# Optimization experiments

Measured on AMD Instinct MI355X. Metric: run time of the kernel, lower is better.

Reference implementation:

```python
import math
import jax, jax.numpy as jnp
import numpy as np

N = 50000      # num nodes
E = 400000     # num edges
IN = 128       # in_channels
HID = 64       # hidden_channels
HEADS = 4
OUT = 32       # out_channels
TDIM = 16      # time_dim
NEG_SLOPE = 0.2
EPS = 1e-5


def setup_inputs() -> dict:
    key = jax.random.key(0)
    ks = jax.random.split(key, 20)
    s = 0.05
    # Fourier time encoder: Linear(1, TDIM) with freq-pattern weight
    freq = np.exp(np.arange(0, TDIM, 2, dtype=np.float32) * -(math.log(10000.0) / TDIM))
    tw = np.zeros((TDIM,), dtype=np.float32)
    tw[0::2] = freq
    tw[1::2] = freq
    return {
        "x": jax.random.normal(ks[0], (N, IN), jnp.float32),
        "edge_index": jax.random.randint(ks[1], (2, E), 0, N, jnp.int64),
        "edge_time": jax.random.uniform(ks[2], (E,), jnp.float32),
        "time_w": jnp.asarray(tw),
        "time_b": jax.random.normal(ks[3], (TDIM,), jnp.float32) * s,
        "proj_w": jax.random.normal(ks[4], (IN + TDIM, IN), jnp.float32) * s,
        "proj_b": jax.random.normal(ks[5], (IN,), jnp.float32) * s,
        "W1": jax.random.normal(ks[6], (IN, HEADS * HID), jnp.float32) * s,
        "a_src1": jax.random.normal(ks[7], (HEADS, HID), jnp.float32) * s,
        "a_dst1": jax.random.normal(ks[8], (HEADS, HID), jnp.float32) * s,
        "b1": jax.random.normal(ks[9], (HEADS * HID,), jnp.float32) * s,
        "g1": jnp.ones((HEADS * HID,), jnp.float32),
        "be1": jnp.zeros((HEADS * HID,), jnp.float32),
        "W2": jax.random.normal(ks[10], (HEADS * HID, OUT), jnp.float32) * s,
        "a_src2": jax.random.normal(ks[11], (1, OUT), jnp.float32) * s,
        "a_dst2": jax.random.normal(ks[12], (1, OUT), jnp.float32) * s,
        "b2": jax.random.normal(ks[13], (OUT,), jnp.float32) * s,
        "g2": jnp.ones((OUT,), jnp.float32),
        "be2": jnp.zeros((OUT,), jnp.float32),
    }


def layer_norm(h, g, b):
    mu = jnp.mean(h, axis=-1, keepdims=True)
    var = jnp.mean(jnp.square(h - mu), axis=-1, keepdims=True)
    return (h - mu) * jax.lax.rsqrt(var + EPS) * g + b


def gat_conv(x, src, dst, W, a_src, a_dst, bias, heads, ch, concat):
    """PyG GATConv (self-loops pre-appended in src/dst), inference (no dropout)."""
    n = x.shape[0]
    h = (x @ W).reshape(n, heads, ch)                       # [N,H,C]
    al_s = jnp.sum(h * a_src, axis=-1)                      # [N,H]
    al_d = jnp.sum(h * a_dst, axis=-1)                      # [N,H]
    e = al_s[src] + al_d[dst]                               # [Etot,H]
    e = jnp.where(e > 0, e, NEG_SLOPE * e)                  # leaky_relu
    m = jax.ops.segment_max(e, dst, num_segments=n)         # scatter-softmax
    ex = jnp.exp(e - m[dst])
    denom = jax.ops.segment_sum(ex, dst, num_segments=n)
    alpha = ex / denom[dst]                                 # [Etot,H]
    out = jax.ops.segment_sum(h[src] * alpha[:, :, None], dst, num_segments=n)  # [N,H,C]
    out = out.reshape(n, heads * ch) if concat else jnp.mean(out, axis=1)
    return out + bias


def reference(x, edge_index, edge_time, time_w, time_b, proj_w, proj_b,
              W1, a_src1, a_dst1, b1, g1, be1,
              W2, a_src2, a_dst2, b2, g2, be2):
    src, dst = edge_index[0], edge_index[1]
    # Fourier time encoding of edge timestamps
    tp = edge_time[:, None] * time_w + time_b               # [E,TDIM]
    even = (jnp.arange(TDIM) % 2) == 0
    t_enc = jnp.where(even, jnp.sin(tp), jnp.cos(tp))       # [E,TDIM]
    # scatter_reduce_(mean, include_self=True) onto source nodes: sum/(count+1)
    t_sum = jax.ops.segment_sum(t_enc, src, num_segments=N)
    cnt = jax.ops.segment_sum(jnp.ones((E,), x.dtype), src, num_segments=N)
    node_time = t_sum / (cnt + 1.0)[:, None]
    xin = jnp.concatenate([x, node_time], axis=-1) @ proj_w + proj_b  # [N,IN]
    # add self loops (PyG GATConv default)
    loop = jnp.arange(N, dtype=src.dtype)
    src2 = jnp.concatenate([src, loop])
    dst2 = jnp.concatenate([dst, loop])
    h = gat_conv(xin, src2, dst2, W1, a_src1, a_dst1, b1, HEADS, HID, True)
    h = jax.nn.elu(h)
    h = layer_norm(h, g1, be1)
    h = gat_conv(h, src2, dst2, W2, a_src2, a_dst2, b2, 1, OUT, False)
    h = layer_norm(h, g2, be2)
    return h
```

## Files before the change

kernel.cpp:

```cpp
#include <hip/hip_runtime.h>
#include <math.h>

#define NN 50000
#define EE 400000
#define INC 128
#define TD 16
#define H1C 256
#define OUTC 32
#define NEG 0.2f
#define PAD 64

typedef _Float16 f16;
typedef __attribute__((ext_vector_type(8))) _Float16 f16x8;
typedef __attribute__((ext_vector_type(2))) _Float16 f16x2;
typedef __attribute__((ext_vector_type(4))) float f32x4;

__device__ __forceinline__ float leaky(float x) { return x > 0.f ? x : NEG * x; }
__device__ __forceinline__ float sel4f(const float4& v, int h) {
  return h == 0 ? v.x : h == 1 ? v.y : h == 2 ? v.z : v.w;
}

__global__ void k_rank(const int* __restrict__ ei, const float* __restrict__ et,
                       int* __restrict__ deg_dst, int* __restrict__ deg_src,
                       int* __restrict__ src_pad, float* __restrict__ et_pad,
                       const float* __restrict__ W1, const float* __restrict__ pw,
                       const float* __restrict__ W2, f16* __restrict__ W1T,
                       f16* __restrict__ pwT, f16* __restrict__ W2T) {
  int gid = blockIdx.x * 256 + threadIdx.x;
  if (gid < EE / 4) {
    int4 sv = *(const int4*)(ei + gid * 4);
    int4 dv = *(const int4*)(ei + EE + gid * 4);
    float4 tv = *(const float4*)(et + gid * 4);
    int rd0 = atomicAdd(&deg_dst[dv.x], 1);
    int rd1 = atomicAdd(&deg_dst[dv.y], 1);
    int rd2 = atomicAdd(&deg_dst[dv.z], 1);
    int rd3 = atomicAdd(&deg_dst[dv.w], 1);
    int rs0 = atomicAdd(&deg_src[sv.x], 1);
    int rs1 = atomicAdd(&deg_src[sv.y], 1);
    int rs2 = atomicAdd(&deg_src[sv.z], 1);
    int rs3 = atomicAdd(&deg_src[sv.w], 1);
    if (rd0 < PAD) src_pad[dv.x * PAD + rd0] = sv.x;
    if (rd1 < PAD) src_pad[dv.y * PAD + rd1] = sv.y;
    if (rd2 < PAD) src_pad[dv.z * PAD + rd2] = sv.z;
    if (rd3 < PAD) src_pad[dv.w * PAD + rd3] = sv.w;
    if (rs0 < PAD) et_pad[sv.x * PAD + rs0] = tv.x;
    if (rs1 < PAD) et_pad[sv.y * PAD + rs1] = tv.y;
    if (rs2 < PAD) et_pad[sv.z * PAD + rs2] = tv.z;
    if (rs3 < PAD) et_pad[sv.w * PAD + rs3] = tv.w;
    return;
  }
  int idx = gid - EE / 4;
  if (idx < 32768) {
    int c = idx >> 7, k = idx & 127;
    W1T[idx] = (f16)W1[k * 256 + c];
  } else if (idx < 53248) {
    int i2 = idx - 32768;
    int c = i2 / 160, kp = i2 - c * 160;
    pwT[i2] = (f16)(kp < 144 ? pw[kp * 128 + c] : 0.f);
  } else if (idx < 61440) {
    int i3 = idx - 53248;
    int c = i3 >> 8, k = i3 & 255;
    W2T[i3] = (f16)W2[k * 32 + c];
  }
}

__global__ void k_time_agg(const int* __restrict__ deg_src,
                           const float* __restrict__ et_pad,
                           const float* __restrict__ tw, const float* __restrict__ tb,
                           float* __restrict__ node_time) {
  int lane = threadIdx.x & 63;
  int n = blockIdx.x * 4 + (threadIdx.x >> 6);
  int cnt = min(deg_src[n], PAD);
  int k = lane & 15, g = lane >> 4;
  float w = tw[k], b = tb[k];
  bool isc = (k & 1);
  float v = 0.f;
  const float* ep = et_pad + (size_t)n * PAD;
  for (int i = g; i < cnt; i += 4) {
    float tp = ep[i] * w + b;
    v += isc ? __cosf(tp) : __sinf(tp);
  }
  v += __shfl_xor(v, 16);
  v += __shfl_xor(v, 32);
  if (lane < 16) node_time[n * TD + k] = v / (float)(cnt + 1);
}

__global__ __launch_bounds__(256) void k_projg(const float* __restrict__ x,
                                               const float* __restrict__ node_time,
                                               const f16* __restrict__ pwT,
                                               const float* __restrict__ pb,
                                               f16* __restrict__ xin) {
  __shared__ f16 A[64 * 168];
  int tid = threadIdx.x, l = tid & 63, w = tid >> 6;
  int n0 = blockIdx.x * 64;
  for (int idx = tid; idx < 64 * 160; idx += 256) {
    int r = idx / 160, c = idx - r * 160;
    int n = n0 + r;
    float v = 0.f;
    if (n < NN) v = (c < 128) ? x[(size_t)n * INC + c]
                              : (c < 144 ? node_time[n * TD + (c - 128)] : 0.f);
    A[r * 168 + c] = (f16)v;
  }
  int r16 = l & 15, g = l >> 4;
  f16x8 breg[2][5];
  #pragma unroll
  for (int jj = 0; jj < 2; ++jj) {
    int col = w * 32 + jj * 16 + r16;
    #pragma unroll
    for (int kk = 0; kk < 5; ++kk)
      breg[jj][kk] = *(const f16x8*)(pwT + col * 160 + kk * 32 + g * 8);
  }
  f32x4 acc[4][2];
  #pragma unroll
  for (int i = 0; i < 4; ++i)
    #pragma unroll
    for (int jj = 0; jj < 2; ++jj) acc[i][jj] = (f32x4){0.f, 0.f, 0.f, 0.f};
  __syncthreads();
  #pragma unroll
  for (int kk = 0; kk < 5; ++kk) {
    #pragma unroll
    for (int i = 0; i < 4; ++i) {
      f16x8 a = *(const f16x8*)(A + (i * 16 + r16) * 168 + kk * 32 + g * 8);
      acc[i][0] = __builtin_amdgcn_mfma_f32_16x16x32_f16(a, breg[0][kk], acc[i][0], 0, 0, 0);
      acc[i][1] = __builtin_amdgcn_mfma_f32_16x16x32_f16(a, breg[1][kk], acc[i][1], 0, 0, 0);
    }
  }
  #pragma unroll
  for (int i = 0; i < 4; ++i)
    #pragma unroll
    for (int jj = 0; jj < 2; ++jj) {
      int col = w * 32 + jj * 16 + r16;
      float bj = pb[col];
      #pragma unroll
      for (int q = 0; q < 4; ++q) {
        int row = n0 + i * 16 + g * 4 + q;
        if (row < NN) xin[(size_t)row * INC + col] = (f16)(acc[i][jj][q] + bj);
      }
    }
}

__global__ __launch_bounds__(256) void k_h1g(const f16* __restrict__ xin,
                                             const f16* __restrict__ W1T,
                                             const float* __restrict__ as1,
                                             const float* __restrict__ ad1,
                                             f16* __restrict__ h1,
                                             float* __restrict__ als,
                                             float* __restrict__ ald) {
  __shared__ f16 A[64 * 136];
  int tid = threadIdx.x, l = tid & 63, w = tid >> 6;
  int n0 = blockIdx.x * 64;
  f16x8 zero = {};
  for (int ci = tid; ci < 1024; ci += 256) {
    int r = ci >> 4, c8 = (ci & 15) * 8;
    int n = n0 + r;
    f16x8 v = (n < NN) ? *(const f16x8*)(xin + (size_t)n * INC + c8) : zero;
    *(f16x8*)(A + r * 136 + c8) = v;
  }
  int r16 = l & 15, g = l >> 4;
  f16x8 breg[4][4];
  #pragma unroll
  for (int jj = 0; jj < 4; ++jj) {
    int col = w * 64 + jj * 16 + r16;
    #pragma unroll
    for (int kk = 0; kk < 4; ++kk)
      breg[jj][kk] = *(const f16x8*)(W1T + col * 128 + kk * 32 + g * 8);
  }
  f32x4 acc[4][4];
  #pragma unroll
  for (int i = 0; i < 4; ++i)
    #pragma unroll
    for (int jj = 0; jj < 4; ++jj) acc[i][jj] = (f32x4){0.f, 0.f, 0.f, 0.f};
  __syncthreads();
  #pragma unroll
  for (int kk = 0; kk < 4; ++kk)
    #pragma unroll
    for (int i = 0; i < 4; ++i) {
      f16x8 a = *(const f16x8*)(A + (i * 16 + r16) * 136 + kk * 32 + g * 8);
      #pragma unroll
      for (int jj = 0; jj < 4; ++jj)
        acc[i][jj] = __builtin_amdgcn_mfma_f32_16x16x32_f16(a, breg[jj][kk], acc[i][jj], 0, 0, 0);
    }
  #pragma unroll
  for (int i = 0; i < 4; ++i)
    #pragma unroll
    for (int jj = 0; jj < 4; ++jj) {
      int col = w * 64 + jj * 16 + r16;
      #pragma unroll
      for (int q = 0; q < 4; ++q) {
        int row = n0 + i * 16 + g * 4 + q;
        if (row < NN) h1[(size_t)row * H1C + col] = (f16)acc[i][jj][q];
      }
    }
  float asc[4], adc[4];
  #pragma unroll
  for (int jj = 0; jj < 4; ++jj) {
    int col = w * 64 + jj * 16 + r16;
    asc[jj] = as1[col];
    adc[jj] = ad1[col];
  }
  #pragma unroll
  for (int i = 0; i < 4; ++i)
    #pragma unroll
    for (int q = 0; q < 4; ++q) {
      float ps = 0.f, pd = 0.f;
      #pragma unroll
      for (int jj = 0; jj < 4; ++jj) {
        ps = fmaf(acc[i][jj][q], asc[jj], ps);
        pd = fmaf(acc[i][jj][q], adc[jj], pd);
      }
      #pragma unroll
      for (int o = 1; o < 16; o <<= 1) {
        ps += __shfl_xor(ps, o);
        pd += __shfl_xor(pd, o);
      }
      int row = n0 + i * 16 + g * 4 + q;
      if (r16 == 0 && row < NN) {
        als[row * 4 + w] = ps;
        ald[row * 4 + w] = pd;
      }
    }
}

__global__ __launch_bounds__(256) void k_h2g(const f16* __restrict__ ln1,
                                             const f16* __restrict__ W2T,
                                             const float* __restrict__ as2,
                                             const float* __restrict__ ad2,
                                             f16* __restrict__ h2,
                                             float* __restrict__ als2,
                                             float* __restrict__ ald2) {
  __shared__ f16 A[64 * 264];
  int tid = threadIdx.x, l = tid & 63, w = tid >> 6;
  int n0 = blockIdx.x * 64;
  f16x8 zero = {};
  for (int ci = tid; ci < 2048; ci += 256) {
    int r = ci >> 5, c8 = (ci & 31) * 8;
    int n = n0 + r;
    f16x8 v = (n < NN) ? *(const f16x8*)(ln1 + (size_t)n * H1C + c8) : zero;
    *(f16x8*)(A + r * 264 + c8) = v;
  }
  int r16 = l & 15, g = l >> 4;
  f16x8 breg[2][8];
  #pragma unroll
  for (int jj = 0; jj < 2; ++jj) {
    int col = jj * 16 + r16;
    #pragma unroll
    for (int kk = 0; kk < 8; ++kk)
      breg[jj][kk] = *(const f16x8*)(W2T + col * 256 + kk * 32 + g * 8);
  }
  f32x4 acc[2];
  acc[0] = (f32x4){0.f, 0.f, 0.f, 0.f};
  acc[1] = (f32x4){0.f, 0.f, 0.f, 0.f};
  __syncthreads();
  #pragma unroll
  for (int kk = 0; kk < 8; ++kk) {
    f16x8 a = *(const f16x8*)(A + (w * 16 + r16) * 264 + kk * 32 + g * 8);
    acc[0] = __builtin_amdgcn_mfma_f32_16x16x32_f16(a, breg[0][kk], acc[0], 0, 0, 0);
    acc[1] = __builtin_amdgcn_mfma_f32_16x16x32_f16(a, breg[1][kk], acc[1], 0, 0, 0);
  }
  #pragma unroll
  for (int jj = 0; jj < 2; ++jj)
    #pragma unroll
    for (int q = 0; q < 4; ++q) {
      int row = n0 + w * 16 + g * 4 + q;
      int col = jj * 16 + r16;
      if (row < NN) h2[(size_t)row * OUTC + col] = (f16)acc[jj][q];
    }
  float as_0 = as2[r16], as_1 = as2[16 + r16];
  float ad_0 = ad2[r16], ad_1 = ad2[16 + r16];
  #pragma unroll
  for (int q = 0; q < 4; ++q) {
    float ps = acc[0][q] * as_0 + acc[1][q] * as_1;
    float pd = acc[0][q] * ad_0 + acc[1][q] * ad_1;
    #pragma unroll
    for (int o = 1; o < 16; o <<= 1) {
      ps += __shfl_xor(ps, o);
      pd += __shfl_xor(pd, o);
    }
    int row = n0 + w * 16 + g * 4 + q;
    if (r16 == 0 && row < NN) {
      als2[row] = ps;
      ald2[row] = pd;
    }
  }
}

__global__ __launch_bounds__(256) void k_agg1(
    const int* __restrict__ deg_dst, const int* __restrict__ src_pad,
    const f16* __restrict__ h1, const float* __restrict__ als,
    const float* __restrict__ ald, const float* __restrict__ b1,
    const float* __restrict__ g1, const float* __restrict__ be1,
    f16* __restrict__ ln1) {
  __shared__ int s_s[8][32];
  __shared__ float s_e[8][128];
  int tid = threadIdx.x;
  int grp = tid >> 5, l32 = tid & 31;
  int n = blockIdx.x * 8 + grp;
  int cnt = min(deg_dst[n], PAD);
  const int* sp = src_pad + (size_t)n * PAD;
  const float4 adv = *(const float4*)(ald + n * 4);
  int hh = l32 >> 3;
  int c0 = l32 * 8;
  float adh = sel4f(adv, hh);
  float seh = __expf(leaky(als[n * 4 + hh] + adh));

  f16x2 accA[4] = {}, accB[4] = {}, accC[4] = {}, accD[4] = {};
  float d = 0.f;
  for (int base = 0; base < cnt; base += 32) {
    int p = base + l32;
    if (p < cnt) {
      int sv = sp[p];
      const float4 a = *(const float4*)(als + sv * 4);
      float4 e4;
      e4.x = __expf(leaky(a.x + adv.x));
      e4.y = __expf(leaky(a.y + adv.y));
      e4.z = __expf(leaky(a.z + adv.z));
      e4.w = __expf(leaky(a.w + adv.w));
      s_s[grp][l32] = sv;
      *(float4*)(&s_e[grp][l32 * 4]) = e4;
    }
    int lim = cnt - base;
    if (lim > 32) lim = 32;
    int j = 0;
    for (; j + 4 <= lim; j += 4) {
      int sA = s_s[grp][j], sB = s_s[grp][j + 1];
      int sC = s_s[grp][j + 2], sD = s_s[grp][j + 3];
      float aA = s_e[grp][j * 4 + hh], aB = s_e[grp][(j + 1) * 4 + hh];
      float aC = s_e[grp][(j + 2) * 4 + hh], aD = s_e[grp][(j + 3) * 4 + hh];
      f16x8 hA = *(const f16x8*)(h1 + (size_t)sA * H1C + c0);
      f16x8 hB = *(const f16x8*)(h1 + (size_t)sB * H1C + c0);
      f16x8 hC = *(const f16x8*)(h1 + (size_t)sC * H1C + c0);
      f16x8 hD = *(const f16x8*)(h1 + (size_t)sD * H1C + c0);
      f16 tA = (f16)aA, tB = (f16)aB, tC = (f16)aC, tD = (f16)aD;
      f16x2 vA = {tA, tA}, vB = {tB, tB}, vC = {tC, tC}, vD = {tD, tD};
      const f16x2* pA = (const f16x2*)&hA;
      const f16x2* pB = (const f16x2*)&hB;
      const f16x2* pC = (const f16x2*)&hC;
      const f16x2* pD = (const f16x2*)&hD;
      #pragma unroll
      for (int k = 0; k < 4; ++k) {
        accA[k] = pA[k] * vA + accA[k];
        accB[k] = pB[k] * vB + accB[k];
        accC[k] = pC[k] * vC + accC[k];
        accD[k] = pD[k] * vD + accD[k];
      }
      d += (aA + aB) + (aC + aD);
    }
    for (; j + 2 <= lim; j += 2) {
      int sA = s_s[grp][j], sB = s_s[grp][j + 1];
      float aA = s_e[grp][j * 4 + hh], aB = s_e[grp][(j + 1) * 4 + hh];
      f16x8 hA = *(const f16x8*)(h1 + (size_t)sA * H1C + c0);
      f16x8 hB = *(const f16x8*)(h1 + (size_t)sB * H1C + c0);
      f16 tA = (f16)aA, tB = (f16)aB;
      f16x2 vA = {tA, tA}, vB = {tB, tB};
      const f16x2* pA = (const f16x2*)&hA;
      const f16x2* pB = (const f16x2*)&hB;
      #pragma unroll
      for (int k = 0; k < 4; ++k) {
        accA[k] = pA[k] * vA + accA[k];
        accB[k] = pB[k] * vB + accB[k];
      }
      d += aA + aB;
    }
    if (j < lim) {
      int sA = s_s[grp][j];
      float aA = s_e[grp][j * 4 + hh];
      f16x8 hA = *(const f16x8*)(h1 + (size_t)sA * H1C + c0);
      f16 tA = (f16)aA;
      f16x2 vA = {tA, tA};
      const f16x2* pA = (const f16x2*)&hA;
      #pragma unroll
      for (int k = 0; k < 4; ++k) accA[k] = pA[k] * vA + accA[k];
      d += aA;
    }
  }
  d += seh;
  float invd = __builtin_amdgcn_rcpf(d);
  f16x8 hv = *(const f16x8*)(h1 + (size_t)n * H1C + c0);
  const f16* fa = (const f16*)accA;
  const f16* fb = (const f16*)accB;
  const f16* fc = (const f16*)accC;
  const f16* fd = (const f16*)accD;
  float4 ba = *(const float4*)(b1 + c0), bb = *(const float4*)(b1 + c0 + 4);
  float v[8];
  #pragma unroll
  for (int u = 0; u < 8; ++u) {
    float bu = u < 4 ? (&ba.x)[u] : (&bb.x)[u - 4];
    float sum = ((float)fa[u] + (float)fb[u]) + ((float)fc[u] + (float)fd[u]);
    float t = fmaf((float)hv[u], seh, sum);
    t = fmaf(t, invd, bu);
    v[u] = t > 0.f ? t : (__expf(t) - 1.f);
  }
  float s1 = 0.f, s2 = 0.f;
  #pragma unroll
  for (int u = 0; u < 8; ++u) { s1 += v[u]; s2 += v[u] * v[u]; }
  #pragma unroll
  for (int o = 16; o >= 1; o >>= 1) {
    s1 += __shfl_xor(s1, o, 32);
    s2 += __shfl_xor(s2, o, 32);
  }
  float mu = s1 * (1.f / 256.f);
  float var = s2 * (1.f / 256.f) - mu * mu;
  float sc = rsqrtf(var + 1e-5f);
  float4 ga = *(const float4*)(g1 + c0), gb = *(const float4*)(g1 + c0 + 4);
  float4 ea = *(const float4*)(be1 + c0), eb = *(const float4*)(be1 + c0 + 4);
  f16x8 o8;
  #pragma unroll
  for (int u = 0; u < 8; ++u) {
    float gu = u < 4 ? (&ga.x)[u] : (&gb.x)[u - 4];
    float eu = u < 4 ? (&ea.x)[u] : (&eb.x)[u - 4];
    o8[u] = (f16)((v[u] - mu) * sc * gu + eu);
  }
  *(f16x8*)(ln1 + (size_t)n * H1C + c0) = o8;
}

__global__ __launch_bounds__(256) void k_agg2(
    const int* __restrict__ deg_dst, const int* __restrict__ src_pad,
    const f16* __restrict__ h2, const float* __restrict__ als2,
    const float* __restrict__ ald2, const float* __restrict__ b2,
    const float* __restrict__ g2, const float* __restrict__ be2,
    float* __restrict__ out) {
  int tid = threadIdx.x;
  int n = blockIdx.x * 8 + (tid >> 5);
  int ch = tid & 31;
  int cnt = min(deg_dst[n], PAD);
  const int* sp = src_pad + (size_t)n * PAD;
  float adn = ald2[n];
  float se = __expf(leaky(als2[n] + adn));
  float acc0 = (float)h2[(size_t)n * OUTC + ch] * se;
  float acc1 = 0.f, acc2 = 0.f, acc3 = 0.f;
  float d0 = se, d1 = 0.f, d2 = 0.f, d3 = 0.f;
  int i = 0;
  for (; i + 4 <= cnt; i += 4) {
    int s0 = sp[i], s1v = sp[i + 1], s2v = sp[i + 2], s3v = sp[i + 3];
    float e0 = __expf(leaky(als2[s0] + adn));
    float e1 = __expf(leaky(als2[s1v] + adn));
    float e2 = __expf(leaky(als2[s2v] + adn));
    float e3 = __expf(leaky(als2[s3v] + adn));
    acc0 = fmaf((float)h2[(size_t)s0 * OUTC + ch], e0, acc0);
    acc1 = fmaf((float)h2[(size_t)s1v * OUTC + ch], e1, acc1);
    acc2 = fmaf((float)h2[(size_t)s2v * OUTC + ch], e2, acc2);
    acc3 = fmaf((float)h2[(size_t)s3v * OUTC + ch], e3, acc3);
    d0 += e0; d1 += e1; d2 += e2; d3 += e3;
  }
  for (; i < cnt; ++i) {
    int s0 = sp[i];
    float e0 = __expf(leaky(als2[s0] + adn));
    acc0 = fmaf((float)h2[(size_t)s0 * OUTC + ch], e0, acc0);
    d0 += e0;
  }
  float invd = __builtin_amdgcn_rcpf((d0 + d1) + (d2 + d3));
  float t = fmaf((acc0 + acc1) + (acc2 + acc3), invd, b2[ch]);
  float s1 = t, s2 = t * t;
  #pragma unroll
  for (int o = 16; o >= 1; o >>= 1) {
    s1 += __shfl_xor(s1, o, 32);
    s2 += __shfl_xor(s2, o, 32);
  }
  float mu = s1 * (1.f / 32.f);
  float var = s2 * (1.f / 32.f) - mu * mu;
  float sc = rsqrtf(var + 1e-5f);
  out[(size_t)n * OUTC + ch] = (t - mu) * sc * g2[ch] + be2[ch];
}

extern "C" void kernel_launch(void* const* d_in, const int* in_sizes, int n_in,
                              void* d_out, int out_size, void* d_ws, size_t ws_size,
                              hipStream_t stream) {
  const float* x   = (const float*)d_in[0];
  const int*   ei  = (const int*)d_in[1];
  const float* et  = (const float*)d_in[2];
  const float* tw  = (const float*)d_in[3];
  const float* tb  = (const float*)d_in[4];
  const float* pw  = (const float*)d_in[5];
  const float* pb  = (const float*)d_in[6];
  const float* W1  = (const float*)d_in[7];
  const float* as1 = (const float*)d_in[8];
  const float* ad1 = (const float*)d_in[9];
  const float* b1  = (const float*)d_in[10];
  const float* g1  = (const float*)d_in[11];
  const float* be1 = (const float*)d_in[12];
  const float* W2  = (const float*)d_in[13];
  const float* as2 = (const float*)d_in[14];
  const float* ad2 = (const float*)d_in[15];
  const float* b2  = (const float*)d_in[16];
  const float* g2  = (const float*)d_in[17];
  const float* be2 = (const float*)d_in[18];

  char* ws = (char*)d_ws;
  size_t off = 0;
  auto alloc = [&](size_t bytes) {
    void* p = ws + off;
    off += (bytes + 255) & ~(size_t)255;
    return p;
  };
  float* node_time = (float*)alloc((size_t)NN * TD * 4);
  f16* xin   = (f16*)alloc((size_t)NN * INC * 2);
  f16* h1    = (f16*)alloc((size_t)NN * H1C * 2);
  f16* ln1   = (f16*)alloc((size_t)NN * H1C * 2);
  f16* h2    = (f16*)alloc((size_t)NN * OUTC * 2);
  float* als1v = (float*)alloc((size_t)NN * 4 * 4);
  float* ald1v = (float*)alloc((size_t)NN * 4 * 4);
  float* als2v = (float*)alloc((size_t)NN * 4);
  float* ald2v = (float*)alloc((size_t)NN * 4);
  int*   src_pad = (int*)alloc((size_t)NN * PAD * 4);
  float* et_pad  = (float*)alloc((size_t)NN * PAD * 4);
  f16* W1T = (f16*)alloc(32768 * 2);
  f16* pwT = (f16*)alloc(20480 * 2);
  f16* W2T = (f16*)alloc(8192 * 2);
  int* deg2 = (int*)alloc((size_t)NN * 2 * 4);
  int* deg_dst = deg2;
  int* deg_src = deg2 + NN;

  hipMemsetAsync(deg2, 0, (size_t)NN * 2 * 4, stream);

  const int NT64 = (NN + 63) / 64;
  k_rank<<<(EE / 4 + 61440 + 255) / 256, 256, 0, stream>>>(ei, et, deg_dst, deg_src,
                                                           src_pad, et_pad, W1, pw, W2,
                                                           W1T, pwT, W2T);
  k_time_agg<<<NN / 4, 256, 0, stream>>>(deg_src, et_pad, tw, tb, node_time);
  k_projg<<<NT64, 256, 0, stream>>>(x, node_time, pwT, pb, xin);
  k_h1g<<<NT64, 256, 0, stream>>>(xin, W1T, as1, ad1, h1, als1v, ald1v);
  k_agg1<<<NN / 8, 256, 0, stream>>>(deg_dst, src_pad, h1, als1v, ald1v,
                                     b1, g1, be1, ln1);
  k_h2g<<<NT64, 256, 0, stream>>>(ln1, W2T, as2, ad2, h2, als2v, ald2v);
  k_agg2<<<NN / 8, 256, 0, stream>>>(deg_dst, src_pad, h2, als2v, ald2v,
                                     b2, g2, be2, (float*)d_out);
}
```

Baseline: 184.1 us.

## Split input projection into x-part fused with edge ranking plus time correction

Splits the input projection: the x-dependent part (128 of 144 input rows) now runs inside the edge-ranking kernel as extra blocks, so it does not wait on time aggregation. The 16-dim node-time contribution is computed in the time aggregation kernel and added in place to xin, which removes the separate projection kernel, the node_time buffer and the pwT transpose. This cuts one launch and overlaps the projection GEMM with the atomic ranking work. In exchange, xin gets an extra f16 read-modify-write, the 16x128 dot product runs on scalar FMAs, and rounding xin to f16 twice loses a little precision.

```diff
diff --git a/kernel.cpp b/kernel.cpp
--- a/kernel.cpp
+++ b/kernel.cpp
@@ -10,6 +10,10 @@
 #define NEG 0.2f
 #define PAD 64
 
+#define EB 391
+#define WB 160
+#define PB 782
+
 typedef _Float16 f16;
 typedef __attribute__((ext_vector_type(8))) _Float16 f16x8;
 typedef __attribute__((ext_vector_type(2))) _Float16 f16x2;
@@ -20,56 +24,117 @@
   return h == 0 ? v.x : h == 1 ? v.y : h == 2 ? v.z : v.w;
 }
 
-__global__ void k_rank(const int* __restrict__ ei, const float* __restrict__ et,
-                       int* __restrict__ deg_dst, int* __restrict__ deg_src,
-                       int* __restrict__ src_pad, float* __restrict__ et_pad,
-                       const float* __restrict__ W1, const float* __restrict__ pw,
-                       const float* __restrict__ W2, f16* __restrict__ W1T,
-                       f16* __restrict__ pwT, f16* __restrict__ W2T) {
-  int gid = blockIdx.x * 256 + threadIdx.x;
-  if (gid < EE / 4) {
-    int4 sv = *(const int4*)(ei + gid * 4);
-    int4 dv = *(const int4*)(ei + EE + gid * 4);
-    float4 tv = *(const float4*)(et + gid * 4);
-    int rd0 = atomicAdd(&deg_dst[dv.x], 1);
-    int rd1 = atomicAdd(&deg_dst[dv.y], 1);
-    int rd2 = atomicAdd(&deg_dst[dv.z], 1);
-    int rd3 = atomicAdd(&deg_dst[dv.w], 1);
-    int rs0 = atomicAdd(&deg_src[sv.x], 1);
-    int rs1 = atomicAdd(&deg_src[sv.y], 1);
-    int rs2 = atomicAdd(&deg_src[sv.z], 1);
-    int rs3 = atomicAdd(&deg_src[sv.w], 1);
-    if (rd0 < PAD) src_pad[dv.x * PAD + rd0] = sv.x;
-    if (rd1 < PAD) src_pad[dv.y * PAD + rd1] = sv.y;
-    if (rd2 < PAD) src_pad[dv.z * PAD + rd2] = sv.z;
-    if (rd3 < PAD) src_pad[dv.w * PAD + rd3] = sv.w;
-    if (rs0 < PAD) et_pad[sv.x * PAD + rs0] = tv.x;
-    if (rs1 < PAD) et_pad[sv.y * PAD + rs1] = tv.y;
-    if (rs2 < PAD) et_pad[sv.z * PAD + rs2] = tv.z;
-    if (rs3 < PAD) et_pad[sv.w * PAD + rs3] = tv.w;
+__global__ __launch_bounds__(256) void k_rank_proj(
+    const int* __restrict__ ei, const float* __restrict__ et,
+    int* __restrict__ deg_dst, int* __restrict__ deg_src,
+    int* __restrict__ src_pad, float* __restrict__ et_pad,
+    const float* __restrict__ W1, const float* __restrict__ W2,
+    f16* __restrict__ W1T, f16* __restrict__ W2T,
+    const float* __restrict__ x, const float* __restrict__ pw,
+    const float* __restrict__ pb, f16* __restrict__ xin) {
+  __shared__ f16 A[64 * 136];
+  int tid = threadIdx.x;
+  int b = blockIdx.x;
+  if (b < EB) {
+    int gid = b * 256 + tid;
+    if (gid < EE / 4) {
+      int4 sv = *(const int4*)(ei + gid * 4);
+      int4 dv = *(const int4*)(ei + EE + gid * 4);
+      float4 tv = *(const float4*)(et + gid * 4);
+      int rd0 = atomicAdd(&deg_dst[dv.x], 1);
+      int rd1 = atomicAdd(&deg_dst[dv.y], 1);
+      int rd2 = atomicAdd(&deg_dst[dv.z], 1);
+      int rd3 = atomicAdd(&deg_dst[dv.w], 1);
+      int rs0 = atomicAdd(&deg_src[sv.x], 1);
+      int rs1 = atomicAdd(&deg_src[sv.y], 1);
+      int rs2 = atomicAdd(&deg_src[sv.z], 1);
+      int rs3 = atomicAdd(&deg_src[sv.w], 1);
+      if (rd0 < PAD) src_pad[dv.x * PAD + rd0] = sv.x;
+      if (rd1 < PAD) src_pad[dv.y * PAD + rd1] = sv.y;
+      if (rd2 < PAD) src_pad[dv.z * PAD + rd2] = sv.z;
+      if (rd3 < PAD) src_pad[dv.w * PAD + rd3] = sv.w;
+      if (rs0 < PAD) et_pad[sv.x * PAD + rs0] = tv.x;
+      if (rs1 < PAD) et_pad[sv.y * PAD + rs1] = tv.y;
+      if (rs2 < PAD) et_pad[sv.z * PAD + rs2] = tv.z;
+      if (rs3 < PAD) et_pad[sv.w * PAD + rs3] = tv.w;
+    }
     return;
   }
-  int idx = gid - EE / 4;
-  if (idx < 32768) {
-    int c = idx >> 7, k = idx & 127;
-    W1T[idx] = (f16)W1[k * 256 + c];
-  } else if (idx < 53248) {
-    int i2 = idx - 32768;
-    int c = i2 / 160, kp = i2 - c * 160;
-    pwT[i2] = (f16)(kp < 144 ? pw[kp * 128 + c] : 0.f);
-  } else if (idx < 61440) {
-    int i3 = idx - 53248;
-    int c = i3 >> 8, k = i3 & 255;
-    W2T[i3] = (f16)W2[k * 32 + c];
-  }
-}
-
-__global__ void k_time_agg(const int* __restrict__ deg_src,
-                           const float* __restrict__ et_pad,
-                           const float* __restrict__ tw, const float* __restrict__ tb,
-                           float* __restrict__ node_time) {
-  int lane = threadIdx.x & 63;
-  int n = blockIdx.x * 4 + (threadIdx.x >> 6);
+  if (b < EB + WB) {
+    int idx = (b - EB) * 256 + tid;
+    if (idx < 32768) {
+      int c = idx >> 7, k = idx & 127;
+      W1T[idx] = (f16)W1[k * 256 + c];
+    } else {
+      int i3 = idx - 32768;
+      int c = i3 >> 8, k = i3 & 255;
+      W2T[i3] = (f16)W2[k * 32 + c];
+    }
+    return;
+  }
+  int n0 = (b - EB - WB) * 64;
+  int l = tid & 63, w = tid >> 6;
+  for (int ci = tid; ci < 1024; ci += 256) {
+    int r = ci >> 4, c8 = (ci & 15) * 8;
+    int n = n0 + r;
+    f16x8 hv = {};
+    if (n < NN) {
+      float4 v0 = *(const float4*)(x + (size_t)n * INC + c8);
+      float4 v1 = *(const float4*)(x + (size_t)n * INC + c8 + 4);
+      hv[0] = (f16)v0.x; hv[1] = (f16)v0.y; hv[2] = (f16)v0.z; hv[3] = (f16)v0.w;
+      hv[4] = (f16)v1.x; hv[5] = (f16)v1.y; hv[6] = (f16)v1.z; hv[7] = (f16)v1.w;
+    }
+    *(f16x8*)(A + r * 136 + c8) = hv;
+  }
+  int r16 = l & 15, g = l >> 4;
+  f16x8 breg[2][4];
+  #pragma unroll
+  for (int jj = 0; jj < 2; ++jj) {
+    int col = w * 32 + jj * 16 + r16;
+    #pragma unroll
+    for (int kk = 0; kk < 4; ++kk)
+      #pragma unroll
+      for (int t = 0; t < 8; ++t)
+        breg[jj][kk][t] = (f16)pw[(size_t)(kk * 32 + g * 8 + t) * 128 + col];
+  }
+  f32x4 acc[4][2];
+  #pragma unroll
+  for (int i = 0; i < 4; ++i)
+    #pragma unroll
+    for (int jj = 0; jj < 2; ++jj) acc[i][jj] = (f32x4){0.f, 0.f, 0.f, 0.f};
+  __syncthreads();
+  #pragma unroll
+  for (int kk = 0; kk < 4; ++kk)
+    #pragma unroll
+    for (int i = 0; i < 4; ++i) {
+      f16x8 a = *(const f16x8*)(A + (i * 16 + r16) * 136 + kk * 32 + g * 8);
+      acc[i][0] = __builtin_amdgcn_mfma_f32_16x16x32_f16(a, breg[0][kk], acc[i][0], 0, 0, 0);
+      acc[i][1] = __builtin_amdgcn_mfma_f32_16x16x32_f16(a, breg[1][kk], acc[i][1], 0, 0, 0);
+    }
+  #pragma unroll
+  for (int i = 0; i < 4; ++i)
+    #pragma unroll
+    for (int jj = 0; jj < 2; ++jj) {
+      int col = w * 32 + jj * 16 + r16;
+      float bj = pb[col];
+      #pragma unroll
+      for (int q = 0; q < 4; ++q) {
+        int row = n0 + i * 16 + g * 4 + q;
+        if (row < NN) xin[(size_t)row * INC + col] = (f16)(acc[i][jj][q] + bj);
+      }
+    }
+}
+
+__global__ __launch_bounds__(256) void k_time_add(
+    const int* __restrict__ deg_src, const float* __restrict__ et_pad,
+    const float* __restrict__ tw, const float* __restrict__ tb,
+    const float* __restrict__ pw, f16* __restrict__ xin) {
+  __shared__ float nt[4][16];
+  __shared__ float pwl[2048];
+  int tid = threadIdx.x;
+  for (int i = tid; i < 2048; i += 256) pwl[i] = pw[16384 + i];
+  int lane = tid & 63, wid = tid >> 6;
+  int n = blockIdx.x * 4 + wid;
   int cnt = min(deg_src[n], PAD);
   int k = lane & 15, g = lane >> 4;
   float w = tw[k], b = tb[k];
@@ -82,61 +147,22 @@
   }
   v += __shfl_xor(v, 16);
   v += __shfl_xor(v, 32);
-  if (lane < 16) node_time[n * TD + k] = v / (float)(cnt + 1);
-}
-
-__global__ __launch_bounds__(256) void k_projg(const float* __restrict__ x,
-                                               const float* __restrict__ node_time,
-                                               const f16* __restrict__ pwT,
-                                               const float* __restrict__ pb,
-                                               f16* __restrict__ xin) {
-  __shared__ f16 A[64 * 168];
-  int tid = threadIdx.x, l = tid & 63, w = tid >> 6;
-  int n0 = blockIdx.x * 64;
-  for (int idx = tid; idx < 64 * 160; idx += 256) {
-    int r = idx / 160, c = idx - r * 160;
-    int n = n0 + r;
-    float v = 0.f;
-    if (n < NN) v = (c < 128) ? x[(size_t)n * INC + c]
-                              : (c < 144 ? node_time[n * TD + (c - 128)] : 0.f);
-    A[r * 168 + c] = (f16)v;
-  }
-  int r16 = l & 15, g = l >> 4;
-  f16x8 breg[2][5];
-  #pragma unroll
-  for (int jj = 0; jj < 2; ++jj) {
-    int col = w * 32 + jj * 16 + r16;
-    #pragma unroll
-    for (int kk = 0; kk < 5; ++kk)
-      breg[jj][kk] = *(const f16x8*)(pwT + col * 160 + kk * 32 + g * 8);
-  }
-  f32x4 acc[4][2];
-  #pragma unroll
-  for (int i = 0; i < 4; ++i)
-    #pragma unroll
-    for (int jj = 0; jj < 2; ++jj) acc[i][jj] = (f32x4){0.f, 0.f, 0.f, 0.f};
+  if (lane < 16) nt[wid][k] = v / (float)(cnt + 1);
   __syncthreads();
-  #pragma unroll
-  for (int kk = 0; kk < 5; ++kk) {
-    #pragma unroll
-    for (int i = 0; i < 4; ++i) {
-      f16x8 a = *(const f16x8*)(A + (i * 16 + r16) * 168 + kk * 32 + g * 8);
-      acc[i][0] = __builtin_amdgcn_mfma_f32_16x16x32_f16(a, breg[0][kk], acc[i][0], 0, 0, 0);
-      acc[i][1] = __builtin_amdgcn_mfma_f32_16x16x32_f16(a, breg[1][kk], acc[i][1], 0, 0, 0);
-    }
-  }
-  #pragma unroll
-  for (int i = 0; i < 4; ++i)
-    #pragma unroll
-    for (int jj = 0; jj < 2; ++jj) {
-      int col = w * 32 + jj * 16 + r16;
-      float bj = pb[col];
-      #pragma unroll
-      for (int q = 0; q < 4; ++q) {
-        int row = n0 + i * 16 + g * 4 + q;
-        if (row < NN) xin[(size_t)row * INC + col] = (f16)(acc[i][jj][q] + bj);
-      }
-    }
+  int c0 = lane * 2;
+  float d0 = 0.f, d1 = 0.f;
+  #pragma unroll
+  for (int t = 0; t < 16; ++t) {
+    float ntv = nt[wid][t];
+    d0 = fmaf(ntv, pwl[t * 128 + c0], d0);
+    d1 = fmaf(ntv, pwl[t * 128 + c0 + 1], d1);
+  }
+  f16x2* xp = (f16x2*)(xin + (size_t)n * INC + c0);
+  f16x2 old = *xp;
+  f16x2 nw;
+  nw[0] = (f16)((float)old[0] + d0);
+  nw[1] = (f16)((float)old[1] + d1);
+  *xp = nw;
 }
 
 __global__ __launch_bounds__(256) void k_h1g(const f16* __restrict__ xin,
@@ -492,7 +518,6 @@
     off += (bytes + 255) & ~(size_t)255;
     return p;
   };
-  float* node_time = (float*)alloc((size_t)NN * TD * 4);
   f16* xin   = (f16*)alloc((size_t)NN * INC * 2);
   f16* h1    = (f16*)alloc((size_t)NN * H1C * 2);
   f16* ln1   = (f16*)alloc((size_t)NN * H1C * 2);
@@ -504,7 +529,6 @@
   int*   src_pad = (int*)alloc((size_t)NN * PAD * 4);
   float* et_pad  = (float*)alloc((size_t)NN * PAD * 4);
   f16* W1T = (f16*)alloc(32768 * 2);
-  f16* pwT = (f16*)alloc(20480 * 2);
   f16* W2T = (f16*)alloc(8192 * 2);
   int* deg2 = (int*)alloc((size_t)NN * 2 * 4);
   int* deg_dst = deg2;
@@ -513,11 +537,9 @@
   hipMemsetAsync(deg2, 0, (size_t)NN * 2 * 4, stream);
 
   const int NT64 = (NN + 63) / 64;
-  k_rank<<<(EE / 4 + 61440 + 255) / 256, 256, 0, stream>>>(ei, et, deg_dst, deg_src,
-                                                           src_pad, et_pad, W1, pw, W2,
-                                                           W1T, pwT, W2T);
-  k_time_agg<<<NN / 4, 256, 0, stream>>>(deg_src, et_pad, tw, tb, node_time);
-  k_projg<<<NT64, 256, 0, stream>>>(x, node_time, pwT, pb, xin);
+  k_rank_proj<<<EB + WB + PB, 256, 0, stream>>>(ei, et, deg_dst, deg_src, src_pad,
+                                                et_pad, W1, W2, W1T, W2T, x, pw, pb, xin);
+  k_time_add<<<NN / 4, 256, 0, stream>>>(deg_src, et_pad, tw, tb, pw, xin);
   k_h1g<<<NT64, 256, 0, stream>>>(xin, W1T, as1, ad1, h1, als1v, ald1v);
   k_agg1<<<NN / 8, 256, 0, stream>>>(deg_dst, src_pad, h1, als1v, ald1v,
                                      b1, g1, be1, ln1);
```

Measured after the change: 172.4 us. -6.3%, faster.
